# Kernel optimization log

Hardware: AMD Instinct MI355X
Metric: run time of the kernel (lower is better)

The kernel has to match this reference:

```python
import jax, jax.numpy as jnp
import numpy as np

NEG_SLOPE = 0.2  # PyG GATConv default leaky_relu slope


def gat_conv(x, ei, W, a_src, a_dst, b, heads, ch):
    """One PyG-style GATConv (eval mode, add_self_loops already applied to ei)."""
    N = x.shape[0]
    h = (x @ W).reshape(N, heads, ch)                      # [N,H,C]
    src, dst = ei[0], ei[1]
    al_s = jnp.sum(h * a_src, axis=-1)                     # [N,H]
    al_d = jnp.sum(h * a_dst, axis=-1)                     # [N,H]
    e = jax.nn.leaky_relu(al_s[src] + al_d[dst], NEG_SLOPE)  # [E,H]
    m = jax.ops.segment_max(e, dst, num_segments=N)        # stable softmax over in-edges
    ex = jnp.exp(e - m[dst])
    den = jax.ops.segment_sum(ex, dst, num_segments=N)
    alpha = ex / den[dst]                                  # [E,H]
    msg = alpha[:, :, None] * h[src]                       # [E,H,C]
    out = jax.ops.segment_sum(msg, dst, num_segments=N)    # [N,H,C]
    return out.reshape(N, heads * ch) + b


def setup_inputs() -> dict:
    key = jax.random.key(0)
    ks = jax.random.split(key, 12)
    N, E, D_in, C, H, D_out = 10000, 320000, 256, 128, 4, 64
    HC = H * C

    def glorot(k, shape):
        fan = shape[0] + shape[-1]
        return jax.random.normal(k, shape, dtype=jnp.float32) * np.sqrt(2.0 / fan)

    x = jax.random.normal(ks[0], (N, D_in), dtype=jnp.float32)
    edge_index = jax.random.randint(ks[1], (2, E), 0, N, dtype=jnp.int64)
    return {
        "x": x,
        "edge_index": edge_index,
        "W1": glorot(ks[2], (D_in, HC)),
        "a_src1": glorot(ks[3], (H, C)),
        "a_dst1": glorot(ks[4], (H, C)),
        "b1": jnp.zeros((HC,), dtype=jnp.float32),
        "W2": glorot(ks[5], (HC, HC)),
        "a_src2": glorot(ks[6], (H, C)),
        "a_dst2": glorot(ks[7], (H, C)),
        "b2": jnp.zeros((HC,), dtype=jnp.float32),
        "W3": glorot(ks[8], (HC, D_out)),
        "a_src3": glorot(ks[9], (1, D_out)),
        "a_dst3": glorot(ks[10], (1, D_out)),
        "b3": jnp.zeros((D_out,), dtype=jnp.float32),
    }


def reference(x, edge_index, W1, a_src1, a_dst1, b1, W2, a_src2, a_dst2, b2,
              W3, a_src3, a_dst3, b3):
    N = x.shape[0]
    loops = jnp.arange(N, dtype=edge_index.dtype)
    ei = jnp.concatenate([edge_index, jnp.stack([loops, loops])], axis=1)
    H, C = a_src1.shape
    h = jax.nn.elu(gat_conv(x, ei, W1, a_src1, a_dst1, b1, H, C))
    h = jax.nn.elu(gat_conv(h, ei, W2, a_src2, a_dst2, b2, H, C))
    out = gat_conv(h, ei, W3, a_src3, a_dst3, b3, 1, a_src3.shape[1])
    return out
```

## Files before the change

### kernel.cpp

```cpp
#include <hip/hip_runtime.h>

typedef short bf16x8 __attribute__((ext_vector_type(8)));
typedef float f32x4 __attribute__((ext_vector_type(4)));

__device__ __forceinline__ unsigned short f2bf(float f) {
    unsigned u = __float_as_uint(f);
    unsigned r = (u + 0x7fffu + ((u >> 16) & 1u)) >> 16;
    return (unsigned short)r;
}
__device__ __forceinline__ float bf2f(unsigned short u) {
    return __uint_as_float(((unsigned)u) << 16);
}

__global__ void k_prep(const float* __restrict__ W1, unsigned short* __restrict__ W1T,
                       const float* __restrict__ W2, unsigned short* __restrict__ W2T,
                       const float* __restrict__ W3, unsigned short* __restrict__ W3T,
                       const float* __restrict__ x, unsigned short* __restrict__ xb,
                       int* __restrict__ csr, int Mcap,
                       const int* __restrict__ ei, int E, int* __restrict__ deg,
                       int DIN, int HC, int DOUT, int N)
{
    int i = blockIdx.x * blockDim.x + threadIdx.x;
    int n1 = DIN * HC;
    int n2 = n1 + HC * HC;
    int n3 = n2 + HC * DOUT;
    int n4 = n3 + N * DIN;
    int n5 = n4 + Mcap;
    int n6 = n5 + E;
    if (i < n1) {
        int k = i / HC, n = i - k * HC;
        W1T[n * DIN + k] = f2bf(W1[i]);
    } else if (i < n2) {
        int j = i - n1;
        int k = j / HC, n = j - k * HC;
        W2T[n * HC + k] = f2bf(W2[j]);
    } else if (i < n3) {
        int j = i - n2;
        int k = j / DOUT, n = j - k * DOUT;
        W3T[n * HC + k] = f2bf(W3[j]);
    } else if (i < n4) {
        int j = i - n3;
        xb[j] = f2bf(x[j]);
    } else if (i < n5) {
        csr[i - n4] = -1;
    } else if (i < n6) {
        atomicAdd(&deg[ei[E + (i - n5)]], 1);
    }
}

__global__ void k_scan(const int* __restrict__ deg, int* __restrict__ off,
                       int* __restrict__ cur, int N) {
    __shared__ int sums[1024];
    int t = threadIdx.x;
    int chunk = (N + 1023) >> 10;
    int lo = t * chunk;
    int hi = lo + chunk; if (hi > N) hi = N;
    if (lo > N) lo = N;
    int s = 0;
    for (int i = lo; i < hi; ++i) s += (deg[i] + 4) & ~3;
    sums[t] = s;
    __syncthreads();
    for (int dd = 1; dd < 1024; dd <<= 1) {
        int v = (t >= dd) ? sums[t - dd] : 0;
        __syncthreads();
        sums[t] += v;
        __syncthreads();
    }
    int run = sums[t] - s;
    for (int i = lo; i < hi; ++i) { off[i] = run; cur[i] = run; run += (deg[i] + 4) & ~3; }
    if (t == 1023) off[N] = run;
}
__global__ void k_fill(const int* __restrict__ ei, int E, int N,
                       int* cur, int* __restrict__ csr, int* __restrict__ dstarr) {
    int i = blockIdx.x * blockDim.x + threadIdx.x;
    if (i < E) {
        int s = ei[i], d = ei[E + i];
        int pos = atomicAdd(&cur[d], 1);
        csr[pos] = s;
        dstarr[pos] = d;
    } else if (i < E + N) {
        int nn = i - E;
        int pos = atomicAdd(&cur[nn], 1);
        csr[pos] = nn;
        dstarr[pos] = nn;
    }
}

template <bool OUTBF>
__global__ __launch_bounds__(256) void k_gemm(
    const unsigned short* __restrict__ A, const unsigned short* __restrict__ BT,
    void* __restrict__ D, int M, int K, int Nc, int tiles_n)
{
    int wid = blockIdx.x * (blockDim.x >> 6) + (threadIdx.x >> 6);
    int tiles_m = (M + 63) >> 6;
    if (wid >= tiles_m * tiles_n) return;
    int lane = threadIdx.x & 63;
    int tm = wid / tiles_n, tn = wid - tm * tiles_n;
    int m0 = tm << 6, n0 = tn << 6;
    int r = lane & 15, q = lane >> 4;

    const unsigned short* Arow[4];
    const unsigned short* Brow[4];
#pragma unroll
    for (int i = 0; i < 4; ++i) {
        int row = m0 + 16 * i + r; row = row < M ? row : M - 1;
        Arow[i] = A + (size_t)row * K + q * 8;
        Brow[i] = BT + (size_t)(n0 + 16 * i + r) * K + q * 8;
    }

    f32x4 acc[4][4] = {};
    bf16x8 a[4], b[4], a2[4], b2[4];
#pragma unroll
    for (int i = 0; i < 4; ++i) {
        a[i] = *(const bf16x8*)(Arow[i]);
        b[i] = *(const bf16x8*)(Brow[i]);
    }
    for (int k0 = 0; k0 < K; k0 += 32) {
        int kn = k0 + 32;
        if (kn < K) {
#pragma unroll
            for (int i = 0; i < 4; ++i) {
                a2[i] = *(const bf16x8*)(Arow[i] + kn);
                b2[i] = *(const bf16x8*)(Brow[i] + kn);
            }
        }
#pragma unroll
        for (int i = 0; i < 4; ++i)
#pragma unroll
            for (int j = 0; j < 4; ++j)
                acc[i][j] = __builtin_amdgcn_mfma_f32_16x16x32_bf16(a[i], b[j], acc[i][j], 0, 0, 0);
        if (kn < K) {
#pragma unroll
            for (int i = 0; i < 4; ++i) { a[i] = a2[i]; b[i] = b2[i]; }
        }
    }
#pragma unroll
    for (int i = 0; i < 4; ++i) {
        int rowb = m0 + 16 * i + q * 4;
#pragma unroll
        for (int rr = 0; rr < 4; ++rr) {
            int row = rowb + rr;
            if (row < M) {
#pragma unroll
                for (int j = 0; j < 4; ++j) {
                    int col = n0 + 16 * j + r;
                    if (OUTBF)
                        ((unsigned short*)D)[(size_t)row * Nc + col] = f2bf(acc[i][j][rr]);
                    else
                        ((float*)D)[(size_t)row * Nc + col] = acc[i][j][rr];
                }
            }
        }
    }
}

template <int HCt, int Ht>
__global__ __launch_bounds__(256) void k_al(
    const unsigned short* __restrict__ h, const float* __restrict__ asrc,
    const float* __restrict__ adst,
    float* __restrict__ als, float* __restrict__ ald, int N)
{
    int wid = blockIdx.x * (blockDim.x >> 6) + (threadIdx.x >> 6);
    if (wid >= N) return;
    int lane = threadIdx.x & 63;
    const int CH = HCt / 64;
    const int Gs = 64 / Ht;
    float s = 0.f, d = 0.f;
    if constexpr (CH == 8) {
        const uint4* hr = (const uint4*)(h + (size_t)wid * HCt) + lane;
        uint4 hv = *hr;
        unsigned wds[4] = {hv.x, hv.y, hv.z, hv.w};
        const f32x4* as4 = (const f32x4*)(asrc + lane * 8);
        const f32x4* ad4 = (const f32x4*)(adst + lane * 8);
        f32x4 av0 = as4[0], av1 = as4[1], dv0 = ad4[0], dv1 = ad4[1];
        float hf[8];
#pragma unroll
        for (int wv = 0; wv < 4; ++wv) {
            hf[2 * wv]     = __uint_as_float(wds[wv] << 16);
            hf[2 * wv + 1] = __uint_as_float(wds[wv] & 0xffff0000u);
        }
#pragma unroll
        for (int j = 0; j < 4; ++j) {
            s += hf[j] * av0[j] + hf[4 + j] * av1[j];
            d += hf[j] * dv0[j] + hf[4 + j] * dv1[j];
        }
    } else {
        float hv = bf2f(h[(size_t)wid * HCt + lane]);
        s = hv * asrc[lane];
        d = hv * adst[lane];
    }
#pragma unroll
    for (int dd = 1; dd < Gs; dd <<= 1) {
        s += __shfl_xor(s, dd);
        d += __shfl_xor(d, dd);
    }
    if ((lane & (Gs - 1)) == 0) {
        int hh = lane / Gs;
        als[wid * Ht + hh] = s;
        ald[wid * Ht + hh] = d;
    }
}

__global__ void k_alpha4(const float* __restrict__ als, const float* __restrict__ ald,
                         const int* __restrict__ csr, const int* __restrict__ dstarr,
                         const int* __restrict__ off, int N,
                         float* __restrict__ alpha, int Mcap)
{
    int t = blockIdx.x * blockDim.x + threadIdx.x;
    if (t >= off[N]) return;
    int s = csr[t];
    if (s < 0) {
#pragma unroll
        for (int h = 0; h < 4; ++h) alpha[(size_t)h * Mcap + t] = 0.f;
        return;
    }
    int d = dstarr[t];
    f32x4 a = *(const f32x4*)(als + (size_t)s * 4);
    f32x4 b = *(const f32x4*)(ald + (size_t)d * 4);
#pragma unroll
    for (int h = 0; h < 4; ++h) {
        float l = a[h] + b[h];
        l = l > 0.f ? l : 0.2f * l;
        alpha[(size_t)h * Mcap + t] = __expf(l);
    }
}

template <bool DOELU>
__global__ __launch_bounds__(256) void k_aggr4b(
    const unsigned short* __restrict__ h, const float* __restrict__ alpha,
    const int* __restrict__ off, const int* __restrict__ csr,
    const float* __restrict__ bias,
    unsigned short* __restrict__ outp, int N, int nodeBlocks, int Mcap)
{
    int head = blockIdx.x / nodeBlocks;
    int nb = blockIdx.x - head * nodeBlocks;
    int n = nb * 4 + (threadIdx.x >> 6);
    if (n >= N) return;
    int lane = threadIdx.x & 63;
    int g = lane >> 4;
    int p = lane & 15;
    int q0 = (off[n] >> 2) + g, q1 = off[n + 1] >> 2;

    float acc[8] = {};
    float den = 0.f;
    const unsigned short* hbase = h + head * 128 + p * 8;
    const int4* csr4 = (const int4*)csr;
    const f32x4* al4 = (const f32x4*)(alpha + (size_t)head * Mcap);

    auto fmaq = [&](float a, const uint4& hq) {
        unsigned wds[4] = {hq.x, hq.y, hq.z, hq.w};
#pragma unroll
        for (int wv = 0; wv < 4; ++wv) {
            acc[2 * wv]     += a * __uint_as_float(wds[wv] << 16);
            acc[2 * wv + 1] += a * __uint_as_float(wds[wv] & 0xffff0000u);
        }
    };

    for (int q = q0; q < q1; q += 4) {
        int4 cs = csr4[q];
        f32x4 av = al4[q];
        int c0 = cs.x < 0 ? 0 : cs.x;
        int c1 = cs.y < 0 ? 0 : cs.y;
        int c2 = cs.z < 0 ? 0 : cs.z;
        int c3 = cs.w < 0 ? 0 : cs.w;
        uint4 h0 = *(const uint4*)(hbase + ((size_t)(unsigned)c0 << 9));
        uint4 h1 = *(const uint4*)(hbase + ((size_t)(unsigned)c1 << 9));
        uint4 h2 = *(const uint4*)(hbase + ((size_t)(unsigned)c2 << 9));
        uint4 h3 = *(const uint4*)(hbase + ((size_t)(unsigned)c3 << 9));
        den += (av[0] + av[1]) + (av[2] + av[3]);
        fmaq(av[0], h0);
        fmaq(av[1], h1);
        fmaq(av[2], h2);
        fmaq(av[3], h3);
    }

    den += __shfl_xor(den, 16);
    den += __shfl_xor(den, 32);
#pragma unroll
    for (int j = 0; j < 8; ++j) {
        acc[j] += __shfl_xor(acc[j], 16);
        acc[j] += __shfl_xor(acc[j], 32);
    }

    if (g == 0) {
        float inv = 1.f / den;
        int cb = head * 128 + p * 8;
        unsigned ww[4];
#pragma unroll
        for (int wv = 0; wv < 4; ++wv) {
            float v0 = acc[2 * wv] * inv + bias[cb + 2 * wv];
            float v1 = acc[2 * wv + 1] * inv + bias[cb + 2 * wv + 1];
            if (DOELU) {
                v0 = v0 > 0.f ? v0 : expm1f(v0);
                v1 = v1 > 0.f ? v1 : expm1f(v1);
            }
            ww[wv] = (unsigned)f2bf(v0) | ((unsigned)f2bf(v1) << 16);
        }
        uint4 o; o.x = ww[0]; o.y = ww[1]; o.z = ww[2]; o.w = ww[3];
        *((uint4*)(outp + (size_t)n * 512 + cb)) = o;
    }
}

__global__ __launch_bounds__(256) void k_aggr1b(
    const unsigned short* __restrict__ h, const float* __restrict__ als,
    const float* __restrict__ aldv, const int* __restrict__ off,
    const int* __restrict__ csr, const float* __restrict__ bias,
    float* __restrict__ outp, int N)
{
    int n = blockIdx.x * (blockDim.x >> 6) + (threadIdx.x >> 6);
    if (n >= N) return;
    int lane = threadIdx.x & 63;
    int g = lane >> 4;
    int p = lane & 15;
    int q0 = (off[n] >> 2) + g, q1 = off[n + 1] >> 2;
    float aldh = aldv[n];

    float acc[4] = {};
    float den = 0.f;
    const unsigned short* hbase = h + p * 4;
    const int4* csr4 = (const int4*)csr;

    auto aof = [&](int ss) -> float {
        int sc = ss < 0 ? 0 : ss;
        float l = als[sc] + aldh;
        l = l > 0.f ? l : 0.2f * l;
        float e = __expf(l);
        return ss < 0 ? 0.f : e;
    };
    auto fmaq = [&](float a, const uint2& hq) {
        den += a;
        acc[0] += a * __uint_as_float(hq.x << 16);
        acc[1] += a * __uint_as_float(hq.x & 0xffff0000u);
        acc[2] += a * __uint_as_float(hq.y << 16);
        acc[3] += a * __uint_as_float(hq.y & 0xffff0000u);
    };

    for (int q = q0; q < q1; q += 4) {
        int4 cs = csr4[q];
        float a0 = aof(cs.x), a1 = aof(cs.y), a2 = aof(cs.z), a3 = aof(cs.w);
        uint2 h0 = *(const uint2*)(hbase + ((size_t)(unsigned)(cs.x < 0 ? 0 : cs.x) << 6));
        uint2 h1 = *(const uint2*)(hbase + ((size_t)(unsigned)(cs.y < 0 ? 0 : cs.y) << 6));
        uint2 h2 = *(const uint2*)(hbase + ((size_t)(unsigned)(cs.z < 0 ? 0 : cs.z) << 6));
        uint2 h3 = *(const uint2*)(hbase + ((size_t)(unsigned)(cs.w < 0 ? 0 : cs.w) << 6));
        fmaq(a0, h0);
        fmaq(a1, h1);
        fmaq(a2, h2);
        fmaq(a3, h3);
    }

    den += __shfl_xor(den, 16);
    den += __shfl_xor(den, 32);
#pragma unroll
    for (int j = 0; j < 4; ++j) {
        acc[j] += __shfl_xor(acc[j], 16);
        acc[j] += __shfl_xor(acc[j], 32);
    }
    if (g == 0) {
        float inv = 1.f / den;
        f32x4 o;
#pragma unroll
        for (int j = 0; j < 4; ++j)
            o[j] = acc[j] * inv + bias[p * 4 + j];
        *((f32x4*)(outp + (size_t)n * 64 + p * 4)) = o;
    }
}

extern "C" void kernel_launch(void* const* d_in, const int* in_sizes, int n_in,
                              void* d_out, int out_size, void* d_ws, size_t ws_size,
                              hipStream_t stream)
{
    const float* x   = (const float*)d_in[0];
    const int*   ei  = (const int*)d_in[1];
    const float* W1  = (const float*)d_in[2];
    const float* as1 = (const float*)d_in[3];
    const float* ad1 = (const float*)d_in[4];
    const float* b1  = (const float*)d_in[5];
    const float* W2  = (const float*)d_in[6];
    const float* as2 = (const float*)d_in[7];
    const float* ad2 = (const float*)d_in[8];
    const float* b2  = (const float*)d_in[9];
    const float* W3  = (const float*)d_in[10];
    const float* as3 = (const float*)d_in[11];
    const float* ad3 = (const float*)d_in[12];
    const float* b3  = (const float*)d_in[13];

    const int DIN = 256, HC = 512, DOUT = 64;
    int N = in_sizes[0] / DIN;
    int E = in_sizes[1] / 2;
    int Mcap = E + 4 * N;

    char* w = (char*)d_ws;
    auto alloc = [&](size_t bytes) -> char* {
        char* p = w;
        w += (bytes + 255) & ~(size_t)255;
        return p;
    };
    int* deg    = (int*)alloc((size_t)N * 4);
    int* cur    = (int*)alloc((size_t)N * 4);
    int* off    = (int*)alloc((size_t)(N + 1) * 4);
    int* csr    = (int*)alloc((size_t)Mcap * 4);
    int* dstarr = (int*)alloc((size_t)Mcap * 4);
    unsigned short* W1T = (unsigned short*)alloc((size_t)HC * DIN * 2);
    unsigned short* W2T = (unsigned short*)alloc((size_t)HC * HC * 2);
    unsigned short* W3T = (unsigned short*)alloc((size_t)DOUT * HC * 2);
    unsigned short* xb  = (unsigned short*)alloc((size_t)N * DIN * 2);
    unsigned short* act = (unsigned short*)alloc((size_t)N * HC * 2);
    unsigned short* hb  = (unsigned short*)alloc((size_t)N * HC * 2);
    unsigned short* hb3 = (unsigned short*)alloc((size_t)N * DOUT * 2);
    float* als   = (float*)alloc((size_t)N * 4 * 4);
    float* ald   = (float*)alloc((size_t)N * 4 * 4);
    float* alpha = (float*)alloc((size_t)Mcap * 4 * 4);

    hipMemsetAsync(deg, 0, (size_t)N * 4, stream);
    int prep_total = DIN * HC + HC * HC + HC * DOUT + N * DIN + Mcap + E;
    k_prep<<<(prep_total + 255) / 256, 256, 0, stream>>>(
        W1, W1T, W2, W2T, W3, W3T, x, xb, csr, Mcap, ei, E, deg, DIN, HC, DOUT, N);
    k_scan<<<1, 1024, 0, stream>>>(deg, off, cur, N);
    k_fill<<<(E + N + 255) / 256, 256, 0, stream>>>(ei, E, N, cur, csr, dstarr);

    int tiles_m = (N + 63) / 64;
    auto gemm_blocks = [&](int tn) { return (tiles_m * tn + 3) / 4; };
    int nwave_blocks = (N + 3) / 4;
    int nodeBlocks = (N + 3) / 4;
    int alpha_blocks = (Mcap + 255) / 256;

    k_gemm<true><<<gemm_blocks(HC / 64), 256, 0, stream>>>(xb, W1T, hb, N, DIN, HC, HC / 64);
    k_al<512, 4><<<nwave_blocks, 256, 0, stream>>>(hb, as1, ad1, als, ald, N);
    k_alpha4<<<alpha_blocks, 256, 0, stream>>>(als, ald, csr, dstarr, off, N, alpha, Mcap);
    k_aggr4b<true><<<4 * nodeBlocks, 256, 0, stream>>>(hb, alpha, off, csr, b1, act, N, nodeBlocks, Mcap);

    k_gemm<true><<<gemm_blocks(HC / 64), 256, 0, stream>>>(act, W2T, hb, N, HC, HC, HC / 64);
    k_al<512, 4><<<nwave_blocks, 256, 0, stream>>>(hb, as2, ad2, als, ald, N);
    k_alpha4<<<alpha_blocks, 256, 0, stream>>>(als, ald, csr, dstarr, off, N, alpha, Mcap);
    k_aggr4b<true><<<4 * nodeBlocks, 256, 0, stream>>>(hb, alpha, off, csr, b2, act, N, nodeBlocks, Mcap);

    k_gemm<true><<<gemm_blocks(1), 256, 0, stream>>>(act, W3T, hb3, N, HC, DOUT, 1);
    k_al<64, 1><<<nwave_blocks, 256, 0, stream>>>(hb3, as3, ad3, als, ald, N);
    k_aggr1b<<<nwave_blocks, 256, 0, stream>>>(hb3, als, ald, off, csr, b3, (float*)d_out, N);
}
```

Measured before the change: 313.9 us.

## Add LDS-staged MFMA GEMM using direct global-to-LDS loads for layers 1-2

Adds a new GEMM kernel that stages 128x32 A tiles and 64x32 B tiles in shared memory through global_load_lds, so the four waves of a block share the loaded tiles. Each wave computes a 64x32 sub-tile with bf16 MFMA. It replaces the older per-wave GEMM for the first two layers and aims to cut redundant global loads. The kernel has no double buffering and issues two barriers per K step, so load latency is exposed, and the larger tile means fewer blocks.

After: 289.2 us. -7.9%, faster.

```diff
diff --git a/kernel.cpp b/kernel.cpp
--- a/kernel.cpp
+++ b/kernel.cpp
@@ -10,6 +10,12 @@
 }
 __device__ __forceinline__ float bf2f(unsigned short u) {
     return __uint_as_float(((unsigned)u) << 16);
+}
+
+__device__ __forceinline__ void gload_lds16(const void* g, void* l) {
+    __builtin_amdgcn_global_load_lds(
+        (const __attribute__((address_space(1))) unsigned int*)g,
+        (__attribute__((address_space(3))) unsigned int*)l, 16, 0, 0);
 }
 
 __global__ void k_prep(const float* __restrict__ W1, unsigned short* __restrict__ W1T,
@@ -154,6 +160,68 @@
     }
 }
 
+__global__ __launch_bounds__(256) void k_gemm_lds(
+    const unsigned short* __restrict__ A, const unsigned short* __restrict__ BT,
+    unsigned short* __restrict__ D, int M, int K, int Nc, int tiles_n)
+{
+    __shared__ unsigned short As[128 * 32];
+    __shared__ unsigned short Bs[64 * 32];
+    int tm = blockIdx.x / tiles_n, tn = blockIdx.x - tm * tiles_n;
+    int m0 = tm << 7, n0 = tn << 6;
+    int tid = threadIdx.x;
+    int w = tid >> 6, lane = tid & 63;
+    int wr = w >> 1, wc = w & 1;
+    int r = lane & 15, q = lane >> 4;
+
+    int lrow = lane >> 2;
+    int lch = (lane & 3) * 8;
+    int ga0 = m0 + w * 16 + lrow;       if (ga0 >= M) ga0 = M - 1;
+    int ga1 = m0 + (w + 4) * 16 + lrow; if (ga1 >= M) ga1 = M - 1;
+    const unsigned short* pa0 = A + (size_t)ga0 * K + lch;
+    const unsigned short* pa1 = A + (size_t)ga1 * K + lch;
+    const unsigned short* pb  = BT + (size_t)(n0 + w * 16 + lrow) * K + lch;
+    unsigned short* lA0 = As + w * 512;
+    unsigned short* lA1 = As + (w + 4) * 512;
+    unsigned short* lB  = Bs + w * 512;
+
+    const unsigned short* arp = As + (wr * 64 + r) * 32 + q * 8;
+    const unsigned short* brp = Bs + (wc * 32 + r) * 32 + q * 8;
+
+    f32x4 acc[4][2] = {};
+    for (int k0 = 0; k0 < K; k0 += 32) {
+        gload_lds16(pa0 + k0, lA0);
+        gload_lds16(pa1 + k0, lA1);
+        gload_lds16(pb + k0, lB);
+        __syncthreads();
+        bf16x8 a[4], b[2];
+#pragma unroll
+        for (int i = 0; i < 4; ++i) a[i] = *(const bf16x8*)(arp + i * 16 * 32);
+#pragma unroll
+        for (int j = 0; j < 2; ++j) b[j] = *(const bf16x8*)(brp + j * 16 * 32);
+#pragma unroll
+        for (int i = 0; i < 4; ++i)
+#pragma unroll
+            for (int j = 0; j < 2; ++j)
+                acc[i][j] = __builtin_amdgcn_mfma_f32_16x16x32_bf16(a[i], b[j], acc[i][j], 0, 0, 0);
+        __syncthreads();
+    }
+#pragma unroll
+    for (int i = 0; i < 4; ++i) {
+        int rowb = m0 + wr * 64 + 16 * i + q * 4;
+#pragma unroll
+        for (int rr = 0; rr < 4; ++rr) {
+            int row = rowb + rr;
+            if (row < M) {
+#pragma unroll
+                for (int j = 0; j < 2; ++j) {
+                    int col = n0 + wc * 32 + 16 * j + r;
+                    D[(size_t)row * Nc + col] = f2bf(acc[i][j][rr]);
+                }
+            }
+        }
+    }
+}
+
 template <int HCt, int Ht>
 __global__ __launch_bounds__(256) void k_al(
     const unsigned short* __restrict__ h, const float* __restrict__ asrc,
@@ -420,16 +488,17 @@
 
     int tiles_m = (N + 63) / 64;
     auto gemm_blocks = [&](int tn) { return (tiles_m * tn + 3) / 4; };
+    int tm128 = (N + 127) / 128;
     int nwave_blocks = (N + 3) / 4;
     int nodeBlocks = (N + 3) / 4;
     int alpha_blocks = (Mcap + 255) / 256;
 
-    k_gemm<true><<<gemm_blocks(HC / 64), 256, 0, stream>>>(xb, W1T, hb, N, DIN, HC, HC / 64);
+    k_gemm_lds<<<tm128 * (HC / 64), 256, 0, stream>>>(xb, W1T, hb, N, DIN, HC, HC / 64);
     k_al<512, 4><<<nwave_blocks, 256, 0, stream>>>(hb, as1, ad1, als, ald, N);
     k_alpha4<<<alpha_blocks, 256, 0, stream>>>(als, ald, csr, dstarr, off, N, alpha, Mcap);
     k_aggr4b<true><<<4 * nodeBlocks, 256, 0, stream>>>(hb, alpha, off, csr, b1, act, N, nodeBlocks, Mcap);
 
-    k_gemm<true><<<gemm_blocks(HC / 64), 256, 0, stream>>>(act, W2T, hb, N, HC, HC, HC / 64);
+    k_gemm_lds<<<tm128 * (HC / 64), 256, 0, stream>>>(act, W2T, hb, N, HC, HC, HC / 64);
     k_al<512, 4><<<nwave_blocks, 256, 0, stream>>>(hb, as2, ad2, als, ald, N);
     k_alpha4<<<alpha_blocks, 256, 0, stream>>>(als, ald, csr, dstarr, off, N, alpha, Mcap);
     k_aggr4b<true><<<4 * nodeBlocks, 256, 0, stream>>>(hb, alpha, off, csr, b2, act, N, nodeBlocks, Mcap);
```
